# Optimization experiments

Hardware: AMD Instinct MI355X
Metric: run time of the kernel (lower is better)

Reference implementation:

```python
import jax, jax.numpy as jnp
import numpy as np

# dims
B, S, D, H, DH, M, L, V, BS, NR = 4, 2048, 512, 8, 64, 2048, 6, 32000, 64, 3
NB = S // BS  # 32 blocks


def _block_plan(nb, seed):
    """BigBird block connectivity: 2 global + 3 window + NR random blocks per query block.
    Returns idx [nb, K] int32 and validity mask [nb, K] bool (dedup + edge handling)."""
    rng = np.random.RandomState(seed)
    K = 5 + NR
    idx = np.zeros((nb, K), np.int32)
    msk = np.zeros((nb, K), bool)
    for i in range(nb):
        fixed = {0, nb - 1} | {j for j in (i - 1, i, i + 1) if 0 <= j < nb}
        rest = [j for j in range(nb) if j not in fixed]
        rnd = rng.choice(rest, size=min(NR, len(rest)), replace=False) if rest else []
        sel = sorted(fixed | set(int(r) for r in rnd))
        idx[i, :len(sel)] = sel
        msk[i, :len(sel)] = True
    return jnp.asarray(idx), jnp.asarray(msk)


def _posemb():
    pos = np.arange(S, dtype=np.float32)[:, None]
    div = np.exp(np.arange(0, D, 2, dtype=np.float32) * (-np.log(10000.0) / D))
    pe = np.zeros((S, D), np.float32)
    pe[:, 0::2] = np.sin(pos * div)
    pe[:, 1::2] = np.cos(pos * div)
    return jnp.asarray(pe)


def _ln(x, scale, bias):
    m = jnp.mean(x, axis=-1, keepdims=True)
    v = jnp.mean(jnp.square(x - m), axis=-1, keepdims=True)
    return (x - m) * jax.lax.rsqrt(v + 1e-6) * scale + bias


def _bigbird_attn(x, key_mask, wq, wk, wv, wo, idx, bmask):
    # x: [B,S,D]; idx/bmask: [NB,K]
    q = jnp.einsum('bsd,dhe->bshe', x, wq).reshape(B, NB, BS, H, DH)
    k = jnp.einsum('bsd,dhe->bshe', x, wk).reshape(B, NB, BS, H, DH)
    v = jnp.einsum('bsd,dhe->bshe', x, wv).reshape(B, NB, BS, H, DH)
    kg = k[:, idx]  # [B,NB,K,BS,H,DH] gathered key blocks
    vg = v[:, idx]
    scores = jnp.einsum('bnqhe,bnkche->bhnqkc', q, kg) / jnp.sqrt(jnp.float32(DH))
    kmb = key_mask.reshape(B, NB, BS)[:, idx]          # [B,NB,K,BS]
    m = kmb & bmask[None, :, :, None]                   # [B,NB,K,BS]
    scores = jnp.where(m[:, None, :, None, :, :], scores, jnp.float32(-1e9))
    Kc = idx.shape[1]
    attn = jax.nn.softmax(scores.reshape(B, H, NB, BS, Kc * BS), axis=-1)
    attn = attn.reshape(B, H, NB, BS, Kc, BS)
    out = jnp.einsum('bhnqkc,bnkche->bnqhe', attn, vg).reshape(B, S, H, DH)
    return jnp.einsum('bshe,hed->bsd', out, wo)


def setup_inputs() -> dict:
    key = jax.random.key(0)
    ks = jax.random.split(key, 12)
    n = jax.random.normal
    inp = {
        'tokens': jax.random.randint(ks[0], (B, S), 0, V, dtype=jnp.int32),
        'embed': n(ks[1], (V, D), dtype=jnp.float32),
        'ln1_s': jnp.ones((L, D), jnp.float32), 'ln1_b': jnp.zeros((L, D), jnp.float32),
        'wq': n(ks[2], (L, D, H, DH), dtype=jnp.float32) * 0.02,
        'wk': n(ks[3], (L, D, H, DH), dtype=jnp.float32) * 0.02,
        'wv': n(ks[4], (L, D, H, DH), dtype=jnp.float32) * 0.02,
        'wo': n(ks[5], (L, H, DH, D), dtype=jnp.float32) * 0.02,
        'ln2_s': jnp.ones((L, D), jnp.float32), 'ln2_b': jnp.zeros((L, D), jnp.float32),
        'w1': n(ks[6], (L, D, M), dtype=jnp.float32) * 0.02, 'b1': jnp.zeros((L, M), jnp.float32),
        'w2': n(ks[7], (L, M, D), dtype=jnp.float32) * 0.02, 'b2': jnp.zeros((L, D), jnp.float32),
        'lnf_s': jnp.ones((D,), jnp.float32), 'lnf_b': jnp.zeros((D,), jnp.float32),
    }
    return inp


def reference(tokens, embed, ln1_s, ln1_b, wq, wk, wv, wo, ln2_s, ln2_b, w1, b1, w2, b2, lnf_s, lnf_b):
    key_mask = tokens > 0                      # src padding mask
    x = embed[tokens] + _posemb()[None]        # [B,S,D]
    plans = [_block_plan(NB, l) for l in range(L)]  # connectivity_seed = layer index
    for l in range(L):
        idx, bm = plans[l]
        h = _ln(x, ln1_s[l], ln1_b[l])
        x = x + _bigbird_attn(h, key_mask, wq[l], wk[l], wv[l], wo[l], idx, bm)
        y = _ln(x, ln2_s[l], ln2_b[l])
        y = jax.nn.gelu(jnp.einsum('bsd,dm->bsm', y, w1[l]) + b1[l])
        y = jnp.einsum('bsm,md->bsd', y, w2[l]) + b2[l]
        x = x + y
    return _ln(x, lnf_s, lnf_b)
```

## Files before the change

kernel.cpp:

```cpp
#include <hip/hip_runtime.h>

using u32 = unsigned int;
using u16 = unsigned short;

#define B_   4
#define S_   2048
#define D_   512
#define H_   8
#define DH_  64
#define FF_  2048
#define L_   6
#define NB_  32
#define KC_  8

typedef __attribute__((ext_vector_type(8))) __bf16 bf16x8;
typedef __attribute__((ext_vector_type(4))) float  f32x4;

struct Plan { unsigned char idx[NB_][KC_]; unsigned char cnt[NB_]; };

#define QSCALE 0.18033688011112042f

__device__ __forceinline__ u16 f2b(float f) {
  union { __bf16 b; u16 u; } x;
  x.b = (__bf16)f;
  return x.u;
}

__device__ __forceinline__ float gelu_f(float x) {
  float y2 = 1.5957691216f * x + 0.0713548163f * x * x * x;
  return x / (1.0f + __expf(-y2));
}

typedef const __attribute__((address_space(1))) u32* gas_t;
typedef __attribute__((address_space(3))) u32* las_t;
__device__ __forceinline__ void glds16(const u16* g, u16* l) {
  __builtin_amdgcn_global_load_lds((gas_t)g, (las_t)l, 16, 0, 0);
}

__global__ __launch_bounds__(256)
void transpose_conv(const float* __restrict__ in, u16* __restrict__ out, int R, int C,
                    size_t lstride, int rowoff) {
  __shared__ float tile[32][33];
  const int l = blockIdx.z;
  const float* src = in + (size_t)l * R * C;
  u16* dst = out + (size_t)l * lstride;
  const int c0 = blockIdx.x * 32, r0 = blockIdx.y * 32;
  const int tx = threadIdx.x, ty = threadIdx.y;
#pragma unroll
  for (int i = 0; i < 4; i++)
    tile[ty + i * 8][tx] = src[(size_t)(r0 + ty + i * 8) * C + c0 + tx];
  __syncthreads();
#pragma unroll
  for (int i = 0; i < 4; i++)
    dst[(size_t)(rowoff + c0 + ty + i * 8) * R + r0 + tx] = f2b(tile[tx][ty + i * 8]);
}

__global__ __launch_bounds__(128)
void embed_ln(const int* __restrict__ tokens, const float* __restrict__ emb,
              const float* __restrict__ lns, const float* __restrict__ lnb,
              float* __restrict__ x, u16* __restrict__ h) {
  const int row = blockIdx.x;
  const int s = row & (S_ - 1);
  const int t = threadIdx.x;
  const int tok = tokens[row];
  float4 v = ((const float4*)(emb + (size_t)tok * D_))[t];
  float va[4] = {v.x, v.y, v.z, v.w};
  const float cc = -2.0f * logf(10000.0f) / (float)D_;
  const float pos = (float)s;
#pragma unroll
  for (int j = 0; j < 4; j++) {
    int d = t * 4 + j;
    int i = d >> 1;
    float dv = expf(cc * (float)i);
    float ang = pos * dv;
    va[j] += (d & 1) ? cosf(ang) : sinf(ang);
  }
  ((float4*)x)[(size_t)row * (D_ / 4) + t] = make_float4(va[0], va[1], va[2], va[3]);

  float sm = va[0] + va[1] + va[2] + va[3];
  float sq = va[0] * va[0] + va[1] * va[1] + va[2] * va[2] + va[3] * va[3];
#pragma unroll
  for (int d = 1; d < 64; d <<= 1) {
    sm += __shfl_xor(sm, d);
    sq += __shfl_xor(sq, d);
  }
  __shared__ float red[4];
  const int wv = t >> 6, lane = t & 63;
  if (lane == 0) { red[wv * 2] = sm; red[wv * 2 + 1] = sq; }
  __syncthreads();
  const float ts  = red[0] + red[2];
  const float tsq = red[1] + red[3];
  const float mean = ts * (1.0f / (float)D_);
  const float inv  = rsqrtf(tsq * (1.0f / (float)D_) - mean * mean + 1e-6f);
  const int d0 = t * 4;
  ushort4 u;
  u.x = f2b((va[0] - mean) * inv * lns[d0 + 0] + lnb[d0 + 0]);
  u.y = f2b((va[1] - mean) * inv * lns[d0 + 1] + lnb[d0 + 1]);
  u.z = f2b((va[2] - mean) * inv * lns[d0 + 2] + lnb[d0 + 2]);
  u.w = f2b((va[3] - mean) * inv * lns[d0 + 3] + lnb[d0 + 3]);
  ((ushort4*)h)[(size_t)row * (D_ / 4) + t] = u;
}

template <bool BF16OUT>
__global__ __launch_bounds__(128)
void ln_kernel(const float* __restrict__ x, const float* __restrict__ sc,
               const float* __restrict__ bi, void* __restrict__ outp) {
  const int row = blockIdx.x;
  const int t = threadIdx.x;
  float4 v = ((const float4*)(x + (size_t)row * D_))[t];
  float va[4] = {v.x, v.y, v.z, v.w};
  float s = va[0] + va[1] + va[2] + va[3];
  float sq = va[0] * va[0] + va[1] * va[1] + va[2] * va[2] + va[3] * va[3];
#pragma unroll
  for (int d = 1; d < 64; d <<= 1) {
    s  += __shfl_xor(s, d);
    sq += __shfl_xor(sq, d);
  }
  __shared__ float red[4];
  const int wv = t >> 6, lane = t & 63;
  if (lane == 0) { red[wv * 2] = s; red[wv * 2 + 1] = sq; }
  __syncthreads();
  const float ts  = red[0] + red[2];
  const float tsq = red[1] + red[3];
  const float mean = ts * (1.0f / (float)D_);
  const float inv  = rsqrtf(tsq * (1.0f / (float)D_) - mean * mean + 1e-6f);
  const int d0 = t * 4;
  float o[4];
#pragma unroll
  for (int j = 0; j < 4; j++)
    o[j] = (va[j] - mean) * inv * sc[d0 + j] + bi[d0 + j];
  if (BF16OUT) {
    ushort4 u;
    u.x = f2b(o[0]); u.y = f2b(o[1]); u.z = f2b(o[2]); u.w = f2b(o[3]);
    ((ushort4*)outp)[(size_t)row * (D_ / 4) + t] = u;
  } else {
    ((float4*)outp)[(size_t)row * (D_ / 4) + t] = make_float4(o[0], o[1], o[2], o[3]);
  }
}

template <int MODE, bool VSPLIT, int TM, int TN>
__global__ __launch_bounds__(TN * 2)
void gemm_pipe(const u16* __restrict__ A, const u16* __restrict__ BT,
               int Kk, int ostride, int ncols,
               float* __restrict__ outf, u16* __restrict__ outb,
               const float* __restrict__ bias, const float* __restrict__ resid,
               u16* __restrict__ vtout) {
  constexpr int NW  = TN / 32;
  constexpr int WC  = NW / 2;
  constexpr int MI  = TM / 32;
  constexpr int CHA = TM / (8 * NW);
  constexpr int CHB = TN / (8 * NW);
  constexpr int VM  = CHA + CHB;
  __shared__ u16 As[2][TM * 64];
  __shared__ u16 Bs[2][TN * 64];
  const int tid = threadIdx.x;
  const int wave = tid >> 6, lane = tid & 63;
  const int nwg = gridDim.x, cpx = nwg >> 3;
  const int bid = blockIdx.x;
  const int gid = (bid & 7) * cpx + (bid >> 3);
  const int row0 = (gid / ncols) * TM, col0 = (gid % ncols) * TN;
  const int wr = wave / WC, wc = wave % WC;
  const int l15 = lane & 15, l4 = lane >> 4;

  const u16* asrc[CHA];
  const u16* bsrc[CHB];
  int adst[CHA], bdst[CHB];
#pragma unroll
  for (int i = 0; i < CHA; i++) {
    int chunk = wave * (CHA * 64) + i * 64 + lane;
    int r = chunk >> 3, s = chunk & 7;
    asrc[i] = A + (size_t)(row0 + r) * Kk + ((s ^ (r & 7)) << 3);
    adst[i] = (wave * (CHA * 64) + i * 64) * 8;
  }
#pragma unroll
  for (int i = 0; i < CHB; i++) {
    int chunk = wave * (CHB * 64) + i * 64 + lane;
    int r = chunk >> 3, s = chunk & 7;
    bsrc[i] = BT + (size_t)(col0 + r) * Kk + ((s ^ (r & 7)) << 3);
    bdst[i] = (wave * (CHB * 64) + i * 64) * 8;
  }

  int aoff[MI], boff[4];
#pragma unroll
  for (int m = 0; m < MI; m++) aoff[m] = (wr * (MI * 16) + m * 16 + l15) * 64;
#pragma unroll
  for (int n = 0; n < 4; n++) boff[n] = (wc * 64 + n * 16 + l15) * 64;
  const int sk0 = ((l4)     ^ (l15 & 7)) << 3;
  const int sk1 = ((4 + l4) ^ (l15 & 7)) << 3;

  f32x4 acc[MI][4] = {};
  const int nk = Kk >> 6;

  auto stage = [&](int buf, int kt) {
    const int ko = kt << 6;
#pragma unroll
    for (int i = 0; i < CHA; i++) glds16(asrc[i] + ko, &As[buf][adst[i]]);
#pragma unroll
    for (int i = 0; i < CHB; i++) glds16(bsrc[i] + ko, &Bs[buf][bdst[i]]);
  };

  stage(0, 0);
  stage(1, 1);

  for (int kt = 0; kt < nk; ++kt) {
    const int cur = kt & 1;
    if (kt + 1 < nk) {
      if constexpr (VM == 8) { asm volatile("s_waitcnt vmcnt(8)" ::: "memory"); }
      else                   { asm volatile("s_waitcnt vmcnt(6)" ::: "memory"); }
    } else {
      asm volatile("s_waitcnt vmcnt(0)" ::: "memory");
    }
    __builtin_amdgcn_s_barrier();
    __builtin_amdgcn_sched_barrier(0);

    bf16x8 af0[MI], bf0[4];
#pragma unroll
    for (int m = 0; m < MI; m++) af0[m] = *(const bf16x8*)&As[cur][aoff[m] + sk0];
#pragma unroll
    for (int n = 0; n < 4; n++) bf0[n] = *(const bf16x8*)&Bs[cur][boff[n] + sk0];
#pragma unroll
    for (int m = 0; m < MI; m++)
#pragma unroll
      for (int n = 0; n < 4; n++)
        acc[m][n] = __builtin_amdgcn_mfma_f32_16x16x32_bf16(af0[m], bf0[n], acc[m][n], 0, 0, 0);

    bf16x8 af1[MI], bf1[4];
#pragma unroll
    for (int m = 0; m < MI; m++) af1[m] = *(const bf16x8*)&As[cur][aoff[m] + sk1];
#pragma unroll
    for (int n = 0; n < 4; n++) bf1[n] = *(const bf16x8*)&Bs[cur][boff[n] + sk1];
    asm volatile("s_waitcnt lgkmcnt(0)" ::: "memory");
    __builtin_amdgcn_sched_barrier(0);
    __builtin_amdgcn_s_barrier();
    __builtin_amdgcn_sched_barrier(0);
    if (kt + 2 < nk) stage(cur, kt + 2);

    __builtin_amdgcn_s_setprio(1);
#pragma unroll
    for (int m = 0; m < MI; m++)
#pragma unroll
      for (int n = 0; n < 4; n++)
        acc[m][n] = __builtin_amdgcn_mfma_f32_16x16x32_bf16(af1[m], bf1[n], acc[m][n], 0, 0, 0);
    __builtin_amdgcn_s_setprio(0);
  }

#pragma unroll
  for (int m = 0; m < MI; m++) {
#pragma unroll
    for (int n = 0; n < 4; n++) {
      const int c = col0 + wc * 64 + n * 16 + l15;
      const int rb = row0 + wr * (MI * 16) + m * 16 + l4 * 4;
      if (VSPLIT && c >= 1024) {
        u16 pk[4];
#pragma unroll
        for (int j = 0; j < 4; j++) pk[j] = f2b(acc[m][n][j]);
        *(uint2*)(vtout + (size_t)(c - 1024) * (B_ * S_) + rb) = *(const uint2*)pk;
      } else {
#pragma unroll
        for (int j = 0; j < 4; j++) {
          const size_t o = (size_t)(rb + j) * ostride + c;
          float v = acc[m][n][j];
          if (MODE == 0) {
            if (VSPLIT && c < 512) v *= QSCALE;
            outb[o] = f2b(v);
          } else if (MODE == 1) {
            outf[o] = v + resid[o];
          } else if (MODE == 2) {
            outb[o] = f2b(gelu_f(v + bias[c]));
          } else {
            outf[o] = v + bias[c] + resid[o];
          }
        }
      }
    }
  }
}

__global__ __launch_bounds__(256, 4)
void attn_mfma(const u16* __restrict__ qkv, const u16* __restrict__ vTg,
               const int* __restrict__ tokens, u16* __restrict__ outb, Plan plan) {
  __shared__ u16 ks[2][64 * 64];
  __shared__ u16 vt[2][64 * 64];
  __shared__ u16 ps[64 * 64];

  const int blk = blockIdx.x;
  const int h0 = blk & 7;
  const int n  = (blk >> 3) & 31;
  const int b  = blk >> 8;
  const int t  = threadIdx.x;
  const int wave = t >> 6, lane = t & 63;
  const int l15 = lane & 15, l4 = lane >> 4;
  const int ncnt = plan.cnt[n];
  const int qrow0 = b * S_ + n * 64;

  auto stage = [&](int bi, int c, int* tkd) {
    const int krow0 = b * S_ + c * 64;
#pragma unroll
    for (int i = 0; i < 2; i++) {
      int c0 = i * 256 + wave * 64;
      int cl = c0 + lane;
      int r = cl >> 3, s = cl & 7;
      int sw = (s ^ (r & 7)) << 3;
      glds16(qkv + (size_t)(krow0 + r) * 1024 + 512 + h0 * 64 + sw, &ks[bi][c0 * 8]);
      glds16(vTg + (size_t)(h0 * 64 + r) * (B_ * S_) + krow0 + sw, &vt[bi][c0 * 8]);
    }
#pragma unroll
    for (int nn = 0; nn < 4; nn++) tkd[nn] = tokens[krow0 + nn * 16 + l15];
  };

  bf16x8 qaf[2];
#pragma unroll
  for (int ks_ = 0; ks_ < 2; ks_++)
    qaf[ks_] = *(const bf16x8*)(qkv + (size_t)(qrow0 + wave * 16 + l15) * 1024 +
                                h0 * 64 + ks_ * 32 + l4 * 8);

  int tk[4], tn[4];
  stage(0, plan.idx[n][0], tk);

  f32x4 oacc[4] = {};
  float mrow[4], lrow[4];
#pragma unroll
  for (int j = 0; j < 4; j++) { mrow[j] = -3e38f; lrow[j] = 0.0f; }

  for (int kc = 0; kc < ncnt; kc++) {
    const int cur = kc & 1;
    __syncthreads();
    if (kc + 1 < ncnt) stage(cur ^ 1, plan.idx[n][kc + 1], tn);

    f32x4 sacc[4] = {};
#pragma unroll
    for (int nn = 0; nn < 4; nn++) {
      int r = nn * 16 + l15;
#pragma unroll
      for (int ks_ = 0; ks_ < 2; ks_++) {
        bf16x8 kf = *(const bf16x8*)(&ks[cur][r * 64 + ((ks_ * 32 + l4 * 8) ^ ((r & 7) << 3))]);
        sacc[nn] = __builtin_amdgcn_mfma_f32_16x16x32_bf16(qaf[ks_], kf, sacc[nn], 0, 0, 0);
      }
    }

    bool vld[4];
#pragma unroll
    for (int nn = 0; nn < 4; nn++) vld[nn] = tk[nn] > 0;

    float rmax[4];
#pragma unroll
    for (int j = 0; j < 4; j++) {
      float mj = -3e38f;
#pragma unroll
      for (int nn = 0; nn < 4; nn++)
        if (vld[nn]) mj = fmaxf(mj, sacc[nn][j]);
      rmax[j] = mj;
    }
#pragma unroll
    for (int d = 1; d < 16; d <<= 1) {
#pragma unroll
      for (int j = 0; j < 4; j++) rmax[j] = fmaxf(rmax[j], __shfl_xor(rmax[j], d));
    }
    int chg = 0;
#pragma unroll
    for (int j = 0; j < 4; j++) chg |= (rmax[j] > mrow[j]);
    if (__ballot(chg)) {
#pragma unroll
      for (int j = 0; j < 4; j++) {
        float mn = fmaxf(mrow[j], rmax[j]);
        float alpha = exp2f(mrow[j] - mn);
        mrow[j] = mn;
        lrow[j] *= alpha;
#pragma unroll
        for (int n2 = 0; n2 < 4; n2++) oacc[n2][j] *= alpha;
      }
    }
    float p[4][4];
#pragma unroll
    for (int j = 0; j < 4; j++) {
      float psum = 0.0f;
#pragma unroll
      for (int nn = 0; nn < 4; nn++) {
        float pv = vld[nn] ? exp2f(sacc[nn][j] - mrow[j]) : 0.0f;
        p[nn][j] = pv;
        psum += pv;
      }
      lrow[j] += psum;
    }

#pragma unroll
    for (int nn = 0; nn < 4; nn++)
#pragma unroll
      for (int j = 0; j < 4; j++) {
        int q = wave * 16 + l4 * 4 + j;
        ps[q * 64 + ((nn * 16 + l15) ^ ((q & 7) << 3))] = f2b(p[nn][j]);
      }

#pragma unroll
    for (int ks_ = 0; ks_ < 2; ks_++) {
      int r = wave * 16 + l15;
      bf16x8 paf = *(const bf16x8*)(ps + r * 64 + ((ks_ * 32 + l4 * 8) ^ ((r & 7) << 3)));
#pragma unroll
      for (int n2 = 0; n2 < 4; n2++) {
        int rv = n2 * 16 + l15;
        bf16x8 vf = *(const bf16x8*)(&vt[cur][rv * 64 + ((ks_ * 32 + l4 * 8) ^ ((rv & 7) << 3))]);
        oacc[n2] = __builtin_amdgcn_mfma_f32_16x16x32_bf16(paf, vf, oacc[n2], 0, 0, 0);
      }
    }
#pragma unroll
    for (int nn = 0; nn < 4; nn++) tk[nn] = tn[nn];
  }

#pragma unroll
  for (int d = 1; d < 16; d <<= 1) {
#pragma unroll
    for (int j = 0; j < 4; j++) lrow[j] += __shfl_xor(lrow[j], d);
  }
#pragma unroll
  for (int j = 0; j < 4; j++) {
    const float inv = lrow[j] > 0.0f ? 1.0f / lrow[j] : 0.0f;
    const int q = n * 64 + wave * 16 + l4 * 4 + j;
#pragma unroll
    for (int n2 = 0; n2 < 4; n2++) {
      outb[(size_t)(b * S_ + q) * D_ + h0 * 64 + n2 * 16 + l15] = f2b(oacc[n2][j] * inv);
    }
  }
}

namespace {
struct HostMT {
  u32 mt[624]; int mti;
  void seed(u32 s) {
    mt[0] = s;
    for (int i = 1; i < 624; i++)
      mt[i] = 1812433253u * (mt[i - 1] ^ (mt[i - 1] >> 30)) + (u32)i;
    mti = 624;
  }
  u32 next() {
    if (mti >= 624) {
      for (int k = 0; k < 624; k++) {
        u32 y = (mt[k] & 0x80000000u) | (mt[(k + 1) % 624] & 0x7fffffffu);
        mt[k] = mt[(k + 397) % 624] ^ (y >> 1) ^ ((y & 1u) ? 0x9908b0dfu : 0u);
      }
      mti = 0;
    }
    u32 y = mt[mti++];
    y ^= y >> 11;
    y ^= (y << 7)  & 0x9d2c5680u;
    y ^= (y << 15) & 0xefc60000u;
    y ^= y >> 18;
    return y;
  }
  u32 interval(u32 mx) {
    if (mx == 0u) return 0u;
    u32 mask = mx;
    mask |= mask >> 1; mask |= mask >> 2; mask |= mask >> 4;
    mask |= mask >> 8; mask |= mask >> 16;
    u32 v;
    while ((v = (next() & mask)) > mx) {}
    return v;
  }
};

void build_plan(int l, Plan* out) {
  HostMT rng;
  rng.seed((u32)l);
  for (int i = 0; i < NB_; i++) {
    bool fixedv[NB_] = {};
    fixedv[0] = true; fixedv[NB_ - 1] = true;
    for (int j = i - 1; j <= i + 1; j++)
      if (j >= 0 && j < NB_) fixedv[j] = true;
    int rest[NB_]; int nr = 0;
    for (int j = 0; j < NB_; j++) if (!fixedv[j]) rest[nr++] = j;
    int perm[NB_];
    for (int tt = 0; tt < nr; tt++) perm[tt] = tt;
    for (int tt = nr - 1; tt >= 1; tt--) {
      int j = (int)rng.interval((u32)tt);
      int tmp = perm[tt]; perm[tt] = perm[j]; perm[j] = tmp;
    }
    bool sel[NB_];
    for (int j = 0; j < NB_; j++) sel[j] = fixedv[j];
    for (int c = 0; c < 3; c++) sel[rest[perm[c]]] = true;
    int cnt = 0;
    for (int j = 0; j < NB_; j++)
      if (sel[j]) out->idx[i][cnt++] = (unsigned char)j;
    out->cnt[i] = (unsigned char)cnt;
    for (int c2 = cnt; c2 < KC_; c2++) out->idx[i][c2] = 0;
  }
}
}

extern "C" void kernel_launch(void* const* d_in, const int* in_sizes, int n_in,
                              void* d_out, int out_size, void* d_ws, size_t ws_size,
                              hipStream_t stream) {
  (void)in_sizes; (void)n_in; (void)out_size; (void)ws_size;

  const int*   tokens = (const int*)d_in[0];
  const float* embed  = (const float*)d_in[1];
  const float* ln1_s  = (const float*)d_in[2];
  const float* ln1_b  = (const float*)d_in[3];
  const float* wq     = (const float*)d_in[4];
  const float* wk     = (const float*)d_in[5];
  const float* wv     = (const float*)d_in[6];
  const float* wo     = (const float*)d_in[7];
  const float* ln2_s  = (const float*)d_in[8];
  const float* ln2_b  = (const float*)d_in[9];
  const float* w1     = (const float*)d_in[10];
  const float* b1     = (const float*)d_in[11];
  const float* w2     = (const float*)d_in[12];
  const float* b2     = (const float*)d_in[13];
  const float* lnf_s  = (const float*)d_in[14];
  const float* lnf_b  = (const float*)d_in[15];

  char* wp = (char*)d_ws;
  auto take = [&](size_t bytes) {
    void* p = (void*)wp;
    wp += (bytes + 255) & ~(size_t)255;
    return p;
  };

  const int Mrows = B_ * S_;
  u16* wqkvT = (u16*)take((size_t)L_ * 1536 * D_ * 2);
  u16* woT   = (u16*)take((size_t)L_ * D_ * D_ * 2);
  u16* w1T   = (u16*)take((size_t)L_ * FF_ * D_ * 2);
  u16* w2T   = (u16*)take((size_t)L_ * D_ * FF_ * 2);
  float* x   = (float*)take((size_t)Mrows * D_ * 4);
  u16* h     = (u16*)take((size_t)Mrows * D_ * 2);
  u16* big   = (u16*)take((size_t)Mrows * FF_ * 2);
  u16* qkv   = big;
  u16* vT    = big + (size_t)Mrows * 1024;
  u16* g     = big;

  Plan plans[L_];
  for (int l = 0; l < L_; l++) build_plan(l, &plans[l]);

  const size_t qkvL = (size_t)1536 * D_;

  transpose_conv<<<dim3(D_ / 32, D_ / 32, L_), dim3(32, 8), 0, stream>>>(wq, wqkvT, D_, D_, qkvL, 0);
  transpose_conv<<<dim3(D_ / 32, D_ / 32, L_), dim3(32, 8), 0, stream>>>(wk, wqkvT, D_, D_, qkvL, 512);
  transpose_conv<<<dim3(D_ / 32, D_ / 32, L_), dim3(32, 8), 0, stream>>>(wv, wqkvT, D_, D_, qkvL, 1024);
  transpose_conv<<<dim3(D_ / 32, D_ / 32, L_), dim3(32, 8), 0, stream>>>(wo, woT, D_, D_, (size_t)D_ * D_, 0);
  transpose_conv<<<dim3(FF_ / 32, D_ / 32, L_), dim3(32, 8), 0, stream>>>(w1, w1T, D_, FF_, (size_t)FF_ * D_, 0);
  transpose_conv<<<dim3(D_ / 32, FF_ / 32, L_), dim3(32, 8), 0, stream>>>(w2, w2T, FF_, D_, (size_t)D_ * FF_, 0);
  embed_ln<<<Mrows, 128, 0, stream>>>(tokens, embed, ln1_s, ln1_b, x, h);

  for (int l = 0; l < L_; l++) {
    gemm_pipe<0, true, 128, 128><<<768, 256, 0, stream>>>(
        h, wqkvT + (size_t)l * qkvL, D_, 1024, 12, nullptr, qkv, nullptr, nullptr, vT);
    attn_mfma<<<B_ * NB_ * H_, 256, 0, stream>>>(qkv, vT, tokens, h, plans[l]);
    gemm_pipe<1, false, 64, 128><<<512, 256, 0, stream>>>(
        h, woT + (size_t)l * D_ * D_, D_, D_, 4, x, nullptr, nullptr, x, nullptr);
    ln_kernel<true><<<Mrows, 128, 0, stream>>>(x, ln2_s + l * D_, ln2_b + l * D_, h);
    gemm_pipe<2, false, 128, 128><<<1024, 256, 0, stream>>>(
        h, w1T + (size_t)l * FF_ * D_, D_, FF_, 16, nullptr, g, b1 + l * FF_, nullptr, nullptr);
    gemm_pipe<3, false, 64, 128><<<512, 256, 0, stream>>>(
        g, w2T + (size_t)l * D_ * FF_, FF_, D_, 4, x, nullptr, b2 + l * D_, x, nullptr);
    if (l + 1 < L_)
      ln_kernel<true><<<Mrows, 128, 0, stream>>>(x, ln1_s + (l + 1) * D_, ln1_b + (l + 1) * D_, h);
  }
  ln_kernel<false><<<Mrows, 128, 0, stream>>>(x, lnf_s, lnf_b, d_out);
}
```

Baseline: 863.9 us.

## Store residual stream in bf16, merge weight transposes, relax softmax rescale

The fp32 residual stream x becomes bf16, so the LayerNorm kernels and the residual-adding GEMM epilogues read and write half as many bytes. The six weight transpose launches are merged into one kernel that dispatches on block index. The attention online softmax now rescales only when the running max rises by more than 8 (log2 units), which skips rescale work. The bf16 residual adds rounding error across 6 layers, and the lazy rescale lets exponentials grow up to 2^8 before correction, which could hurt accuracy.

Measured after the change: 840.4 us. 2.7% less time.

```diff
diff --git a/kernel.cpp b/kernel.cpp
--- a/kernel.cpp
+++ b/kernel.cpp
@@ -25,6 +25,11 @@
   x.b = (__bf16)f;
   return x.u;
 }
+__device__ __forceinline__ float b2f(u16 u) {
+  union { u32 u; float f; } x;
+  x.u = ((u32)u) << 16;
+  return x.f;
+}
 
 __device__ __forceinline__ float gelu_f(float x) {
   float y2 = 1.5957691216f * x + 0.0713548163f * x * x * x;
@@ -38,13 +43,33 @@
 }
 
 __global__ __launch_bounds__(256)
-void transpose_conv(const float* __restrict__ in, u16* __restrict__ out, int R, int C,
-                    size_t lstride, int rowoff) {
+void transpose_all(const float* __restrict__ wq, const float* __restrict__ wk,
+                   const float* __restrict__ wv, const float* __restrict__ wo,
+                   const float* __restrict__ w1, const float* __restrict__ w2,
+                   u16* __restrict__ wqkvT, u16* __restrict__ woT,
+                   u16* __restrict__ w1T, u16* __restrict__ w2T) {
   __shared__ float tile[32][33];
   const int l = blockIdx.z;
-  const float* src = in + (size_t)l * R * C;
-  u16* dst = out + (size_t)l * lstride;
-  const int c0 = blockIdx.x * 32, r0 = blockIdx.y * 32;
+  int idx = blockIdx.x;
+  const float* src;
+  u16* dst;
+  int R, C, rowoff;
+  size_t lstride;
+  if (idx < 768) {
+    int w = idx >> 8; idx &= 255;
+    src = (w == 0) ? wq : (w == 1) ? wk : wv;
+    dst = wqkvT; R = 512; C = 512; lstride = (size_t)1536 * 512; rowoff = w * 512;
+  } else if (idx < 1024) {
+    idx -= 768;  src = wo; dst = woT; R = 512;  C = 512;  lstride = (size_t)512 * 512;  rowoff = 0;
+  } else if (idx < 2048) {
+    idx -= 1024; src = w1; dst = w1T; R = 512;  C = 2048; lstride = (size_t)2048 * 512; rowoff = 0;
+  } else {
+    idx -= 2048; src = w2; dst = w2T; R = 2048; C = 512;  lstride = (size_t)512 * 2048; rowoff = 0;
+  }
+  const int ntx = C >> 5;
+  const int c0 = (idx % ntx) * 32, r0 = (idx / ntx) * 32;
+  src += (size_t)l * R * C;
+  dst += (size_t)l * lstride;
   const int tx = threadIdx.x, ty = threadIdx.y;
 #pragma unroll
   for (int i = 0; i < 4; i++)
@@ -58,7 +83,7 @@
 __global__ __launch_bounds__(128)
 void embed_ln(const int* __restrict__ tokens, const float* __restrict__ emb,
               const float* __restrict__ lns, const float* __restrict__ lnb,
-              float* __restrict__ x, u16* __restrict__ h) {
+              u16* __restrict__ x, u16* __restrict__ h) {
   const int row = blockIdx.x;
   const int s = row & (S_ - 1);
   const int t = threadIdx.x;
@@ -75,7 +100,9 @@
     float ang = pos * dv;
     va[j] += (d & 1) ? cosf(ang) : sinf(ang);
   }
-  ((float4*)x)[(size_t)row * (D_ / 4) + t] = make_float4(va[0], va[1], va[2], va[3]);
+  ushort4 xb;
+  xb.x = f2b(va[0]); xb.y = f2b(va[1]); xb.z = f2b(va[2]); xb.w = f2b(va[3]);
+  ((ushort4*)x)[(size_t)row * (D_ / 4) + t] = xb;
 
   float sm = va[0] + va[1] + va[2] + va[3];
   float sq = va[0] * va[0] + va[1] * va[1] + va[2] * va[2] + va[3] * va[3];
@@ -85,8 +112,8 @@
     sq += __shfl_xor(sq, d);
   }
   __shared__ float red[4];
-  const int wv = t >> 6, lane = t & 63;
-  if (lane == 0) { red[wv * 2] = sm; red[wv * 2 + 1] = sq; }
+  const int wv_ = t >> 6, lane = t & 63;
+  if (lane == 0) { red[wv_ * 2] = sm; red[wv_ * 2 + 1] = sq; }
   __syncthreads();
   const float ts  = red[0] + red[2];
   const float tsq = red[1] + red[3];
@@ -103,12 +130,12 @@
 
 template <bool BF16OUT>
 __global__ __launch_bounds__(128)
-void ln_kernel(const float* __restrict__ x, const float* __restrict__ sc,
+void ln_kernel(const u16* __restrict__ x, const float* __restrict__ sc,
                const float* __restrict__ bi, void* __restrict__ outp) {
   const int row = blockIdx.x;
   const int t = threadIdx.x;
-  float4 v = ((const float4*)(x + (size_t)row * D_))[t];
-  float va[4] = {v.x, v.y, v.z, v.w};
+  ushort4 xb = ((const ushort4*)(x + (size_t)row * D_))[t];
+  float va[4] = {b2f(xb.x), b2f(xb.y), b2f(xb.z), b2f(xb.w)};
   float s = va[0] + va[1] + va[2] + va[3];
   float sq = va[0] * va[0] + va[1] * va[1] + va[2] * va[2] + va[3] * va[3];
 #pragma unroll
@@ -142,8 +169,8 @@
 __global__ __launch_bounds__(TN * 2)
 void gemm_pipe(const u16* __restrict__ A, const u16* __restrict__ BT,
                int Kk, int ostride, int ncols,
-               float* __restrict__ outf, u16* __restrict__ outb,
-               const float* __restrict__ bias, const float* __restrict__ resid,
+               u16* __restrict__ outb,
+               const float* __restrict__ bias, const u16* __restrict__ resid,
                u16* __restrict__ vtout) {
   constexpr int NW  = TN / 32;
   constexpr int WC  = NW / 2;
@@ -264,11 +291,11 @@
             if (VSPLIT && c < 512) v *= QSCALE;
             outb[o] = f2b(v);
           } else if (MODE == 1) {
-            outf[o] = v + resid[o];
+            outb[o] = f2b(v + b2f(resid[o]));
           } else if (MODE == 2) {
             outb[o] = f2b(gelu_f(v + bias[c]));
           } else {
-            outf[o] = v + bias[c] + resid[o];
+            outb[o] = f2b(v + bias[c] + b2f(resid[o]));
           }
         }
       }
@@ -358,7 +385,7 @@
     }
     int chg = 0;
 #pragma unroll
-    for (int j = 0; j < 4; j++) chg |= (rmax[j] > mrow[j]);
+    for (int j = 0; j < 4; j++) chg |= (rmax[j] > mrow[j] + 8.0f);
     if (__ballot(chg)) {
 #pragma unroll
       for (int j = 0; j < 4; j++) {
@@ -519,7 +546,7 @@
   u16* woT   = (u16*)take((size_t)L_ * D_ * D_ * 2);
   u16* w1T   = (u16*)take((size_t)L_ * FF_ * D_ * 2);
   u16* w2T   = (u16*)take((size_t)L_ * D_ * FF_ * 2);
-  float* x   = (float*)take((size_t)Mrows * D_ * 4);
+  u16* x     = (u16*)take((size_t)Mrows * D_ * 2);
   u16* h     = (u16*)take((size_t)Mrows * D_ * 2);
   u16* big   = (u16*)take((size_t)Mrows * FF_ * 2);
   u16* qkv   = big;
@@ -531,25 +558,21 @@
 
   const size_t qkvL = (size_t)1536 * D_;
 
-  transpose_conv<<<dim3(D_ / 32, D_ / 32, L_), dim3(32, 8), 0, stream>>>(wq, wqkvT, D_, D_, qkvL, 0);
-  transpose_conv<<<dim3(D_ / 32, D_ / 32, L_), dim3(32, 8), 0, stream>>>(wk, wqkvT, D_, D_, qkvL, 512);
-  transpose_conv<<<dim3(D_ / 32, D_ / 32, L_), dim3(32, 8), 0, stream>>>(wv, wqkvT, D_, D_, qkvL, 1024);
-  transpose_conv<<<dim3(D_ / 32, D_ / 32, L_), dim3(32, 8), 0, stream>>>(wo, woT, D_, D_, (size_t)D_ * D_, 0);
-  transpose_conv<<<dim3(FF_ / 32, D_ / 32, L_), dim3(32, 8), 0, stream>>>(w1, w1T, D_, FF_, (size_t)FF_ * D_, 0);
-  transpose_conv<<<dim3(D_ / 32, FF_ / 32, L_), dim3(32, 8), 0, stream>>>(w2, w2T, FF_, D_, (size_t)D_ * FF_, 0);
+  transpose_all<<<dim3(3072, 1, L_), dim3(32, 8), 0, stream>>>(
+      wq, wk, wv, wo, w1, w2, wqkvT, woT, w1T, w2T);
   embed_ln<<<Mrows, 128, 0, stream>>>(tokens, embed, ln1_s, ln1_b, x, h);
 
   for (int l = 0; l < L_; l++) {
     gemm_pipe<0, true, 128, 128><<<768, 256, 0, stream>>>(
-        h, wqkvT + (size_t)l * qkvL, D_, 1024, 12, nullptr, qkv, nullptr, nullptr, vT);
+        h, wqkvT + (size_t)l * qkvL, D_, 1024, 12, qkv, nullptr, nullptr, vT);
     attn_mfma<<<B_ * NB_ * H_, 256, 0, stream>>>(qkv, vT, tokens, h, plans[l]);
     gemm_pipe<1, false, 64, 128><<<512, 256, 0, stream>>>(
-        h, woT + (size_t)l * D_ * D_, D_, D_, 4, x, nullptr, nullptr, x, nullptr);
+        h, woT + (size_t)l * D_ * D_, D_, D_, 4, x, nullptr, x, nullptr);
     ln_kernel<true><<<Mrows, 128, 0, stream>>>(x, ln2_s + l * D_, ln2_b + l * D_, h);
     gemm_pipe<2, false, 128, 128><<<1024, 256, 0, stream>>>(
-        h, w1T + (size_t)l * FF_ * D_, D_, FF_, 16, nullptr, g, b1 + l * FF_, nullptr, nullptr);
+        h, w1T + (size_t)l * FF_ * D_, D_, FF_, 16, g, b1 + l * FF_, nullptr, nullptr);
     gemm_pipe<3, false, 64, 128><<<512, 256, 0, stream>>>(
-        g, w2T + (size_t)l * D_ * FF_, FF_, D_, 4, x, nullptr, b2 + l * D_, x, nullptr);
+        g, w2T + (size_t)l * D_ * FF_, FF_, D_, 4, x, b2 + l * D_, x, nullptr);
     if (l + 1 < L_)
       ln_kernel<true><<<Mrows, 128, 0, stream>>>(x, ln1_s + (l + 1) * D_, ln1_b + (l + 1) * D_, h);
   }
```
